# Optimization experiments

Hardware: AMD Instinct MI355X
Metric: run time of the kernel (lower is better)

Reference implementation:

```python
import jax, jax.numpy as jnp
import numpy as np

B, S, H, NH, E, D = 2, 2048, 1024, 16, 8, 1024
HD = H // NH
EPS = 1e-5


def act_quant(x):
    # BitNet b1.58 per-row (last axis) int8 activation quant with STE
    s = 127.0 / jnp.clip(jnp.max(jnp.abs(x), axis=-1, keepdims=True), 1e-5, None)
    q = jnp.clip(jnp.round(x * s), -128, 127) / s
    return x + jax.lax.stop_gradient(q - x)


def w_quant(w, axes=None):
    # ternary weight quant (mean-abs scale) with STE; axes=None -> whole tensor
    s = 1.0 / jnp.clip(jnp.mean(jnp.abs(w), axis=axes, keepdims=axes is not None), 1e-5, None)
    q = jnp.clip(jnp.round(w * s), -1, 1) / s
    return w + jax.lax.stop_gradient(q - w)


def bitlinear(x, w):  # x [..., I], w [O, I] (torch layout)
    return act_quant(x) @ w_quant(w).T


def rmsnorm(x, w):
    return x * jax.lax.rsqrt(jnp.mean(x * x, axis=-1, keepdims=True) + EPS) * w


def setup_inputs() -> dict:
    key = jax.random.key(0)
    ks = jax.random.split(key, 10)
    def n(k, shape, scale=0.02):
        return jax.random.normal(k, shape, jnp.float32) * scale
    return {
        "x": jax.random.normal(ks[0], (B, S, H), jnp.float32),
        "q_w": n(ks[1], (H, H)),
        "k_w": n(ks[2], (H, H)),
        "v_w": n(ks[3], (H, H)),
        "o_w": n(ks[4], (H, H)),
        "ln1_w": jnp.ones((H,), jnp.float32),
        "ln2_w": jnp.ones((H,), jnp.float32),
        "router_w": n(ks[5], (E, H)),
        "gate_w": n(ks[6], (E, D, H)),
        "up_w": n(ks[7], (E, D, H)),
        "down_w": n(ks[8], (E, H, D)),
    }


def reference(x, q_w, k_w, v_w, o_w, ln1_w, ln2_w, router_w, gate_w, up_w, down_w):
    # ---- attention (BitNet projections, manual causal softmax) ----
    residual = x
    xn = rmsnorm(x, ln1_w)
    q = bitlinear(xn, q_w).reshape(B, S, NH, HD).transpose(0, 2, 1, 3)  # [B,NH,S,HD]
    k = bitlinear(xn, k_w).reshape(B, S, NH, HD).transpose(0, 2, 1, 3)
    v = bitlinear(xn, v_w).reshape(B, S, NH, HD).transpose(0, 2, 1, 3)
    scale = 1.0 / jnp.sqrt(jnp.asarray(HD, x.dtype))
    attn = jnp.einsum('bhqd,bhkd->bhqk', q, k) * scale
    causal = jnp.triu(jnp.ones((S, S), bool), k=1)
    attn = jnp.where(causal[None, None], -jnp.inf, attn)
    attn = jax.nn.softmax(attn, axis=-1)
    h = jnp.einsum('bhqk,bhkd->bhqd', attn, v).transpose(0, 2, 1, 3).reshape(B, S, H)
    x = residual + bitlinear(h, o_w)

    # ---- top-1 MoE (BitNet experts, relu^2 glu) ----
    residual = x
    xn = rmsnorm(x, ln2_w)
    xf = xn.reshape(-1, H)                       # [T, H], T = B*S
    logits = xf @ router_w.T                     # [T, E]
    idx = jnp.argmax(logits, axis=-1)            # [T]
    onehot = jax.nn.one_hot(idx, E, dtype=x.dtype)  # [T, E]

    xq = act_quant(xf)
    gw = w_quant(gate_w, axes=(1, 2))            # per-expert ternary
    uw = w_quant(up_w, axes=(1, 2))
    dw = w_quant(down_w, axes=(1, 2))
    g = jnp.einsum('th,edh->etd', xq, gw)        # [E, T, D]
    u = jnp.einsum('th,edh->etd', xq, uw)
    hh = jnp.square(jnp.maximum(g, 0)) * u       # relu(gate)^2 * up
    o = jnp.einsum('etd,ehd->eth', act_quant(hh), dw)  # [E, T, H]
    moe = jnp.einsum('eth,te->th', o, onehot).reshape(B, S, H)

    return residual + moe
```

## Files before the change

### kernel.cpp

```cpp
#include <hip/hip_runtime.h>
#include <stdint.h>
#include <math.h>

#define NTOK 4096
#define H    1024
#define NHEAD 16
#define HD   64
#define SEQ  2048
#define NE   8
#define DDIM 1024

typedef __attribute__((ext_vector_type(4)))  int i32x4;
typedef __attribute__((ext_vector_type(16))) int i32x16;
typedef __attribute__((ext_vector_type(8)))  short bf16x8;
typedef __attribute__((ext_vector_type(4)))  float f32x4;


__device__ __forceinline__ i32x16 mfma_i8(i32x4 a, i32x4 b, i32x16 c) {
  return __builtin_amdgcn_mfma_i32_32x32x32_i8(a, b, c, 0, 0, 0);
}

__device__ __forceinline__ unsigned int f2bf(float f) {
  unsigned int u = __float_as_uint(f);
  return (u + 0x7fffu + ((u >> 16) & 1u)) >> 16;
}
__device__ __forceinline__ float bf2f(unsigned int b) {
  return __uint_as_float(b << 16);
}
__device__ __forceinline__ unsigned int f2bf2hl(float a, float b, unsigned int& lo) {
  unsigned int ha = f2bf(a), hb = f2bf(b);
  lo = f2bf(a - bf2f(ha)) | (f2bf(b - bf2f(hb)) << 16);
  return ha | (hb << 16);
}
__device__ __forceinline__ unsigned int fpair(float a) {
  unsigned int hi = f2bf(a);
  unsigned int lo = f2bf(a - bf2f(hi));
  return hi | (lo << 16);
}
__device__ __forceinline__ unsigned int ror16(unsigned int x) {
  return (x >> 16) | (x << 16);
}

__device__ __forceinline__ double bredd(double v, int op, double* tmp) {
#pragma unroll
  for (int o = 32; o; o >>= 1) {
    double w = __shfl_xor(v, o);
    v = op ? fmax(v, w) : v + w;
  }
  int wid = threadIdx.x >> 6;
  if ((threadIdx.x & 63) == 0) tmp[wid] = v;
  __syncthreads();
  double r = op ? fmax(fmax(tmp[0], tmp[1]), fmax(tmp[2], tmp[3]))
                : (tmp[0] + tmp[1] + tmp[2] + tmp[3]);
  __syncthreads();
  return r;
}

__device__ __forceinline__ int qpackd(double n0, double n1, double n2, double n3, double s) {
  int a = (int)fmin(fmax(rint(n0 * s), -128.0), 127.0);
  int b = (int)fmin(fmax(rint(n1 * s), -128.0), 127.0);
  int c = (int)fmin(fmax(rint(n2 * s), -128.0), 127.0);
  int d = (int)fmin(fmax(rint(n3 * s), -128.0), 127.0);
  return (a & 255) | ((b & 255) << 8) | ((c & 255) << 16) | ((d & 255) << 24);
}

__device__ __forceinline__ const float* wsrc(int tensor,
    const float* qw_, const float* kw_, const float* vw_, const float* ow_,
    const float* gw_, const float* uw_, const float* dw_) {
  if (tensor < 4) return tensor == 0 ? qw_ : tensor == 1 ? kw_ : tensor == 2 ? vw_ : ow_;
  if (tensor < 12) return gw_ + ((long long)(tensor - 4) << 20);
  if (tensor < 20) return uw_ + ((long long)(tensor - 12) << 20);
  return dw_ + ((long long)(tensor - 20) << 20);
}


__global__ __launch_bounds__(256) void k_absum(
    const float* qw_, const float* kw_, const float* vw_, const float* ow_,
    const float* gw_, const float* uw_, const float* dw_, double* partial) {
  __shared__ double tmp[4];
  int tensor = blockIdx.x >> 10;
  int j = ((blockIdx.x & 1023) << 10) + threadIdx.x * 4;
  const float* src = wsrc(tensor, qw_, kw_, vw_, ow_, gw_, uw_, dw_);
  float4 w = *(const float4*)(src + j);
  double v = fabs((double)w.x) + fabs((double)w.y) + fabs((double)w.z) + fabs((double)w.w);
  v = bredd(v, 0, tmp);
  if (threadIdx.x == 0) partial[blockIdx.x] = v;
}

__global__ __launch_bounds__(256) void k_wscale(const double* partial, double* wsd) {
  __shared__ double tmp[4];
  int tensor = blockIdx.x;
  const double* p = partial + (tensor << 10);
  int i = threadIdx.x * 4;
  double v = p[i] + p[i + 1] + p[i + 2] + p[i + 3];
  v = bredd(v, 0, tmp);
  if (threadIdx.x == 0) wsd[tensor] = 1.0 / fmax(v * (1.0 / 1048576.0), 1e-5);
}

__global__ __launch_bounds__(256) void k_quantw(
    const float* qw_, const float* kw_, const float* vw_, const float* ow_,
    const float* gw_, const float* uw_, const float* dw_,
    const double* wsd, int8_t* qw) {
  int tensor = blockIdx.x >> 10;
  int j = ((blockIdx.x & 1023) << 10) + threadIdx.x * 4;
  const float* src = wsrc(tensor, qw_, kw_, vw_, ow_, gw_, uw_, dw_);
  double s = wsd[tensor];
  float4 w = *(const float4*)(src + j);
  int a = (int)fmin(fmax(rint((double)w.x * s), -1.0), 1.0);
  int b = (int)fmin(fmax(rint((double)w.y * s), -1.0), 1.0);
  int c = (int)fmin(fmax(rint((double)w.z * s), -1.0), 1.0);
  int d = (int)fmin(fmax(rint((double)w.w * s), -1.0), 1.0);
  ((int*)qw)[(tensor << 18) + (j >> 2)] =
      (a & 255) | ((b & 255) << 8) | ((c & 255) << 16) | ((d & 255) << 24);
}


__global__ __launch_bounds__(256) void k_rms1(const float* X, const float* lnw,
                                              int8_t* xq, double* xsd) {
  __shared__ double tmp[4];
  int t = blockIdx.x, tid = threadIdx.x;
  float4 xv = ((const float4*)(X + (long long)t * H))[tid];
  double x0 = xv.x, x1 = xv.y, x2 = xv.z, x3 = xv.w;
  double ss = x0 * x0 + x1 * x1 + x2 * x2 + x3 * x3;
  ss = bredd(ss, 0, tmp);
  double r = 1.0 / sqrt(ss * (1.0 / 1024.0) + 1e-5);
  float4 wv = ((const float4*)lnw)[tid];
  double n0 = x0 * r * wv.x, n1 = x1 * r * wv.y, n2 = x2 * r * wv.z, n3 = x3 * r * wv.w;
  double ma = fmax(fmax(fabs(n0), fabs(n1)), fmax(fabs(n2), fabs(n3)));
  ma = bredd(ma, 1, tmp);
  double s = 127.0 / fmax(ma, 1e-5);
  ((int*)xq)[t * 256 + tid] = qpackd(n0, n1, n2, n3, s);
  if (tid == 0) xsd[t] = s;
}

__global__ __launch_bounds__(256) void k_actq(const float* X, int8_t* xq, double* xsd) {
  __shared__ double tmp[4];
  int t = blockIdx.x, tid = threadIdx.x;
  float4 xv = ((const float4*)(X + (long long)t * H))[tid];
  double x0 = xv.x, x1 = xv.y, x2 = xv.z, x3 = xv.w;
  double ma = fmax(fmax(fabs(x0), fabs(x1)), fmax(fabs(x2), fabs(x3)));
  ma = bredd(ma, 1, tmp);
  double s = 127.0 / fmax(ma, 1e-5);
  ((int*)xq)[t * 256 + tid] = qpackd(x0, x1, x2, x3, s);
  if (tid == 0) xsd[t] = s;
}


__global__ __launch_bounds__(256) void k_gemm(
    const int8_t* __restrict__ Xq, const double* __restrict__ xsd,
    const int8_t* __restrict__ W, const double* __restrict__ wsd, int widx,
    const float* __restrict__ residual, float* __restrict__ out) {
  __shared__ i32x4 Xs[4][64];
  __shared__ i32x4 Ws[4][128];
  __shared__ double invs[64];
  int tid = threadIdx.x;
  int t0 = blockIdx.y * 64, n0 = blockIdx.x * 128;
  int w = tid >> 6, lane = tid & 63;
  int lrow = lane & 31, lk = lane >> 5;
  int xrow = tid >> 2, xkc = tid & 3;
  i32x16 acc[2];
#pragma unroll
  for (int i = 0; i < 2; i++)
#pragma unroll
    for (int r = 0; r < 16; r++) acc[i][r] = 0;

  for (int k0 = 0; k0 < 1024; k0 += 64) {
    Xs[xkc][xrow] = *(const i32x4*)(Xq + (long long)(t0 + xrow) * 1024 + k0 + xkc * 16);
#pragma unroll
    for (int i = 0; i < 2; i++) {
      int u = tid * 2 + i;
      int row = u >> 2, kc = u & 3;
      Ws[kc][row] = *(const i32x4*)(W + (long long)(n0 + row) * 1024 + k0 + kc * 16);
    }
    __syncthreads();
#pragma unroll
    for (int ks = 0; ks < 2; ks++) {
      i32x4 a0 = Xs[ks * 2 + lk][lrow];
      i32x4 a1 = Xs[ks * 2 + lk][32 + lrow];
      i32x4 b  = Ws[ks * 2 + lk][w * 32 + lrow];
      acc[0] = mfma_i8(a0, b, acc[0]);
      acc[1] = mfma_i8(a1, b, acc[1]);
    }
    __syncthreads();
  }

  double sw = wsd[widx];
  if (tid < 64) invs[tid] = 1.0 / (xsd[t0 + tid] * sw);
  __syncthreads();
  int n = n0 + w * 32 + lrow;
#pragma unroll
  for (int i = 0; i < 2; i++) {
#pragma unroll
    for (int r = 0; r < 16; r++) {
      int rl = i * 32 + (r & 3) + 8 * (r >> 2) + 4 * lk;
      int trow = t0 + rl;
      double v = (double)acc[i][r] * invs[rl];
      if (residual) v += (double)residual[(long long)trow * H + n];
      out[(long long)trow * H + n] = (float)v;
    }
  }
}


__global__ __launch_bounds__(256) void k_gemm3(
    const int8_t* __restrict__ Xq, const double* __restrict__ xsd,
    const int8_t* __restrict__ qw, const double* __restrict__ wsd,
    float* __restrict__ outq, unsigned short* __restrict__ Kh,
    unsigned short* __restrict__ Kl, unsigned int* __restrict__ Vp) {
  __shared__ i32x4 Xs[4][128];
  __shared__ i32x4 Ws[4][128];
  __shared__ double invs[128];
  int z = blockIdx.z;
  const int8_t* W = qw + ((long long)z << 20);
  int tid = threadIdx.x;
  int t0 = blockIdx.y * 128, n0 = blockIdx.x * 128;
  int w = tid >> 6, lane = tid & 63;
  int wm = w >> 1, wn = w & 1;
  int lrow = lane & 31, lk = lane >> 5;
  i32x16 acc[2][2];
#pragma unroll
  for (int i = 0; i < 2; i++)
#pragma unroll
    for (int j = 0; j < 2; j++)
#pragma unroll
      for (int r = 0; r < 16; r++) acc[i][j][r] = 0;

  for (int k0 = 0; k0 < 1024; k0 += 64) {
#pragma unroll
    for (int i = 0; i < 2; i++) {
      int u = tid * 2 + i;
      int row = u >> 2, kc = u & 3;
      Xs[kc][row] = *(const i32x4*)(Xq + (long long)(t0 + row) * 1024 + k0 + kc * 16);
      Ws[kc][row] = *(const i32x4*)(W  + (long long)(n0 + row) * 1024 + k0 + kc * 16);
    }
    __syncthreads();
#pragma unroll
    for (int ks = 0; ks < 2; ks++) {
      i32x4 a0 = Xs[ks * 2 + lk][wm * 64 + lrow];
      i32x4 a1 = Xs[ks * 2 + lk][wm * 64 + 32 + lrow];
      i32x4 b0 = Ws[ks * 2 + lk][wn * 64 + lrow];
      i32x4 b1 = Ws[ks * 2 + lk][wn * 64 + 32 + lrow];
      acc[0][0] = mfma_i8(a0, b0, acc[0][0]);
      acc[0][1] = mfma_i8(a0, b1, acc[0][1]);
      acc[1][0] = mfma_i8(a1, b0, acc[1][0]);
      acc[1][1] = mfma_i8(a1, b1, acc[1][1]);
    }
    __syncthreads();
  }

  double sw = wsd[z];
  if (tid < 128) invs[tid] = 1.0 / (xsd[t0 + tid] * sw);
  __syncthreads();
#pragma unroll
  for (int i = 0; i < 2; i++) {
#pragma unroll
    for (int r = 0; r < 16; r++) {
      int rloc = wm * 64 + i * 32 + (r & 3) + 8 * (r >> 2) + 4 * lk;
      long long base = (long long)(t0 + rloc) * H;
      double inv = invs[rloc];
#pragma unroll
      for (int j = 0; j < 2; j++) {
        int n = n0 + wn * 64 + j * 32 + lrow;
        float vf = (float)((double)acc[i][j][r] * inv);
        long long idx = base + n;
        if (z == 0) {
          outq[idx] = vf;
        } else if (z == 1) {
          unsigned int h = f2bf(vf);
          unsigned int l = f2bf(vf - bf2f(h));
          Kh[idx] = (unsigned short)h;
          Kl[idx] = (unsigned short)l;
        } else {
          Vp[idx] = fpair(vf);
        }
      }
    }
  }
}


__global__ __launch_bounds__(256) void k_knorm(const unsigned short* __restrict__ Kh,
                                               const unsigned short* __restrict__ Kl,
                                               float* __restrict__ Mk) {
  __shared__ float tmp[4];
  int bh = blockIdx.x;
  int b = bh >> 4, head = bh & 15;
  int tid = threadIdx.x;
  float mx = 0.f;
  for (int key = tid; key < SEQ; key += 256) {
    long long base = ((long long)(b * SEQ + key)) * H + head * HD;
    const uint4* hq4 = (const uint4*)(Kh + base);
    const uint4* lq4 = (const uint4*)(Kl + base);
    float s = 0.f;
#pragma unroll
    for (int i = 0; i < 8; i++) {
      uint4 hu = hq4[i], lu = lq4[i];
      const unsigned int hw[4] = {hu.x, hu.y, hu.z, hu.w};
      const unsigned int lw[4] = {lu.x, lu.y, lu.z, lu.w};
#pragma unroll
      for (int j = 0; j < 4; j++) {
        float v0 = bf2f(hw[j] & 0xffffu) + bf2f(lw[j] & 0xffffu);
        float v1 = bf2f(hw[j] >> 16)     + bf2f(lw[j] >> 16);
        s += v0 * v0 + v1 * v1;
      }
    }
    mx = fmaxf(mx, s);
  }
#pragma unroll
  for (int o = 32; o; o >>= 1) mx = fmaxf(mx, __shfl_xor(mx, o));
  if ((tid & 63) == 0) tmp[tid >> 6] = mx;
  __syncthreads();
  if (tid == 0)
    Mk[bh] = sqrtf(fmaxf(fmaxf(tmp[0], tmp[1]), fmaxf(tmp[2], tmp[3])));
}


__global__ __launch_bounds__(512, 4) void k_attn(
    const float* __restrict__ Q, const unsigned short* __restrict__ KH,
    const unsigned short* __restrict__ KL, const unsigned int* __restrict__ VP,
    float* __restrict__ O, const float* __restrict__ Mk) {
  __shared__ unsigned short Qb[64][72];
  __shared__ unsigned short Ql[64][72];
  __shared__ unsigned short Kb[64][72];
  __shared__ unsigned short Kl[64][72];
  __shared__ unsigned int   VA[64][76];
  __shared__ unsigned int   Pw[64][76];
  __shared__ float mbs[64];
  __shared__ float lsh[8][16];
  int i = blockIdx.x;
  int hb = (i & 7) | (((i >> 3) & 3) << 3);
  int p  = ((i >> 5) & 7) | (((i >> 8) & 1) << 3);
  int head = hb & 15, b = hb >> 4;
  int tid = threadIdx.x;
  int w = tid >> 6, lane = tid & 63;
  int quad = lane >> 2, dp = lane & 3;
  int d0 = dp << 4;
  int l15 = lane & 15, lhi = lane >> 4;
  int qh = w >> 2, ks = w & 3;
  long long bh_base = ((long long)b * SEQ) * H + head * HD;
  float mkv = Mk[b * 16 + head];

  int srow = tid >> 3;
  int sd = (tid & 7) << 3;
  int vswz = (tid & 7) << 2;

  int qb = w >> 1;

  for (int ph = 0; ph < 2; ph++) {
    int g = ph ? (31 - p) : p;
    int qlo = g * 64;

    {
      const float* qg = Q + bh_base + (long long)(qlo + srow) * H + sd;
      float4 a = *(const float4*)qg;
      float4 c = *(const float4*)(qg + 4);
      uint4 phh, pll;
      phh.x = f2bf2hl(a.x * 0.125f, a.y * 0.125f, pll.x);
      phh.y = f2bf2hl(a.z * 0.125f, a.w * 0.125f, pll.y);
      phh.z = f2bf2hl(c.x * 0.125f, c.y * 0.125f, pll.z);
      phh.w = f2bf2hl(c.z * 0.125f, c.w * 0.125f, pll.w);
      *(uint4*)&Qb[srow][sd] = phh;
      *(uint4*)&Ql[srow][sd] = pll;
    }

    if (ks == 0) {
      int j0 = qh * 32 + quad * 2;
#pragma unroll
      for (int qq = 0; qq < 2; qq++) {
        int j = j0 + qq;
        const float4* qp_ = (const float4*)(Q + bh_base + (long long)(qlo + j) * H + d0);
        float ss = 0.f;
#pragma unroll
        for (int i2 = 0; i2 < 4; i2++) {
          float4 t = qp_[i2];
          ss += t.x * t.x + t.y * t.y + t.z * t.z + t.w * t.w;
        }
        ss += __shfl_xor(ss, 1);
        ss += __shfl_xor(ss, 2);
        if (dp == 0) mbs[j] = 0.125f * sqrtf(ss) * mkv;
      }
    }

    float lp[4] = {0.f, 0.f, 0.f, 0.f};
    f32x4 oacc[2];
#pragma unroll
    for (int fi = 0; fi < 2; fi++)
#pragma unroll
      for (int r = 0; r < 4; r++) oacc[fi][r] = 0.f;

    __syncthreads();

    bf16x8 qah[2], qal[2];
#pragma unroll
    for (int ks2 = 0; ks2 < 2; ks2++) {
      qah[ks2] = *(const bf16x8*)&Qb[qb * 16 + l15][ks2 * 32 + lhi * 8];
      qal[ks2] = *(const bf16x8*)&Ql[qb * 16 + l15][ks2 * 32 + lhi * 8];
    }
    float mbr4[4];
#pragma unroll
    for (int r = 0; r < 4; r++) mbr4[r] = mbs[qb * 16 + lhi * 4 + r];

    for (int t = 0; t <= g; t++) {
      {
        long long idx = bh_base + (long long)(t * 64 + srow) * H + sd;
        *(uint4*)&Kb[srow][sd] = *(const uint4*)(KH + idx);
        *(uint4*)&Kl[srow][sd] = *(const uint4*)(KL + idx);
        const uint4* vg = (const uint4*)(VP + idx);
        uint4 va = vg[0], vb = vg[1];
        int col = srow ^ vswz;
        VA[sd + 0][col] = va.x;
        VA[sd + 1][col] = va.y;
        VA[sd + 2][col] = va.z;
        VA[sd + 3][col] = va.w;
        VA[sd + 4][col] = vb.x;
        VA[sd + 5][col] = vb.y;
        VA[sd + 6][col] = vb.z;
        VA[sd + 7][col] = vb.w;
      }
      __syncthreads();

      {
        bool dg = (t == g);
#pragma unroll
        for (int kb2 = 0; kb2 < 2; kb2++) {
          int kb = (w & 1) * 2 + kb2;
          f32x4 c = {0.f, 0.f, 0.f, 0.f};
          __builtin_amdgcn_s_setprio(1);
#pragma unroll
          for (int ks2 = 0; ks2 < 2; ks2++) {
            bf16x8 bh = *(const bf16x8*)&Kb[kb * 16 + l15][ks2 * 32 + lhi * 8];
            bf16x8 bl = *(const bf16x8*)&Kl[kb * 16 + l15][ks2 * 32 + lhi * 8];
            c = __builtin_amdgcn_mfma_f32_16x16x32_bf16(qal[ks2], bh, c, 0, 0, 0);
            c = __builtin_amdgcn_mfma_f32_16x16x32_bf16(qah[ks2], bl, c, 0, 0, 0);
            c = __builtin_amdgcn_mfma_f32_16x16x32_bf16(qah[ks2], bh, c, 0, 0, 0);
          }
          __builtin_amdgcn_s_setprio(0);
          int colc = kb * 16 + l15;
#pragma unroll
          for (int r = 0; r < 4; r++) {
            int row = qb * 16 + lhi * 4 + r;
            float wgt = (dg && colc > row) ? 0.f : __expf(c[r] - mbr4[r]);
            lp[r] += wgt;
            Pw[row][colc] = fpair(wgt);
          }
        }
      }
      __syncthreads();

      __builtin_amdgcn_s_setprio(1);
#pragma unroll
      for (int c4 = 0; c4 < 4; c4++) {
        bf16x8 af = *(const bf16x8*)&Pw[qb * 16 + l15][c4 * 16 + lhi * 4];
#pragma unroll
        for (int fi = 0; fi < 2; fi++) {
          int d4 = (w * 2 + fi) & 3;
          int row = d4 * 16 + l15;
          int rswz = ((row >> 3) & 7) << 2;
          union { uint4 q; unsigned int u[4]; bf16x8 v; } bb, bs;
          bb.q = *(const uint4*)&VA[row][(c4 * 16 + lhi * 4) ^ rswz];
          oacc[fi] = __builtin_amdgcn_mfma_f32_16x16x32_bf16(af, bb.v, oacc[fi], 0, 0, 0);
#pragma unroll
          for (int j = 0; j < 4; j++)
            bs.u[j] = ror16(bb.u[j]);
          oacc[fi] = __builtin_amdgcn_mfma_f32_16x16x32_bf16(af, bs.v, oacc[fi], 0, 0, 0);
        }
      }
      __builtin_amdgcn_s_setprio(0);
      __syncthreads();
    }

#pragma unroll
    for (int r = 0; r < 4; r++) {
      lp[r] += __shfl_xor(lp[r], 1);
      lp[r] += __shfl_xor(lp[r], 2);
      lp[r] += __shfl_xor(lp[r], 4);
      lp[r] += __shfl_xor(lp[r], 8);
    }
    if (l15 == 0) {
#pragma unroll
      for (int r = 0; r < 4; r++) lsh[w][lhi * 4 + r] = lp[r];
    }
    __syncthreads();

#pragma unroll
    for (int fi = 0; fi < 2; fi++) {
      int f = w * 2 + fi;
      int d4 = f & 3;
#pragma unroll
      for (int r = 0; r < 4; r++) {
        int idx = lhi * 4 + r;
        float lt = lsh[qb * 2][idx] + lsh[qb * 2 + 1][idx];
        float inv = 1.f / lt;
        int qrow = qb * 16 + idx;
        O[bh_base + (long long)(qlo + qrow) * H + d4 * 16 + l15] = oacc[fi][r] * inv;
      }
    }
    __syncthreads();
  }
}


__global__ __launch_bounds__(256) void k_rms2_router(
    const float* X2, const float* lnw, const float* rw,
    int8_t* xq, double* xsd, int* eidx) {
  __shared__ double tmp[4];
  __shared__ double xn[1024];
  __shared__ double logits[8];
  int t = blockIdx.x, tid = threadIdx.x;
  float4 xv = ((const float4*)(X2 + (long long)t * H))[tid];
  double x0 = xv.x, x1 = xv.y, x2 = xv.z, x3 = xv.w;
  double ss = x0 * x0 + x1 * x1 + x2 * x2 + x3 * x3;
  ss = bredd(ss, 0, tmp);
  double r = 1.0 / sqrt(ss * (1.0 / 1024.0) + 1e-5);
  float4 wv = ((const float4*)lnw)[tid];
  double n0 = x0 * r * wv.x, n1 = x1 * r * wv.y, n2 = x2 * r * wv.z, n3 = x3 * r * wv.w;
  xn[tid * 4 + 0] = n0; xn[tid * 4 + 1] = n1;
  xn[tid * 4 + 2] = n2; xn[tid * 4 + 3] = n3;
  double ma = fmax(fmax(fabs(n0), fabs(n1)), fmax(fabs(n2), fabs(n3)));
  ma = bredd(ma, 1, tmp);
  double s = 127.0 / fmax(ma, 1e-5);
  ((int*)xq)[t * 256 + tid] = qpackd(n0, n1, n2, n3, s);
  if (tid == 0) xsd[t] = s;
  if (tid < 64) {
    int e = tid >> 3, i = tid & 7;
    const float* wr = rw + e * 1024;
    double p = 0.0;
    for (int h = i; h < 1024; h += 8) p += xn[h] * (double)wr[h];
    p += __shfl_xor(p, 1);
    p += __shfl_xor(p, 2);
    p += __shfl_xor(p, 4);
    if (i == 0) logits[e] = p;
  }
  __syncthreads();
  if (tid == 0) {
    double best = logits[0];
    int bi = 0;
    for (int e = 1; e < 8; e++)
      if (logits[e] > best) { best = logits[e]; bi = e; }
    eidx[t] = bi;
  }
}


__global__ __launch_bounds__(256) void k_route(const int* __restrict__ eidx,
                                               int* __restrict__ meta,
                                               int* __restrict__ tokidx) {
  __shared__ int cnt[8], pb[9], cur[8];
  int tid = threadIdx.x;
  if (tid < 8) cnt[tid] = 0;
  __syncthreads();
  for (int t = tid; t < NTOK; t += 256) atomicAdd(&cnt[eidx[t]], 1);
  __syncthreads();
  if (tid == 0) {
    pb[0] = 0;
    int nt = 0;
    for (int e = 0; e < 8; e++) {
      int tiles = (cnt[e] + 63) >> 6;
      for (int i = 0; i < tiles; i++) meta[1 + nt + i] = e;
      nt += tiles;
      pb[e + 1] = pb[e] + tiles * 64;
      cur[e] = pb[e];
    }
    meta[0] = nt;
  }
  __syncthreads();
  for (int s = tid; s < 4608; s += 256) tokidx[s] = -1;
  __syncthreads();
  for (int t = tid; t < NTOK; t += 256) {
    int e = eidx[t];
    int s = atomicAdd(&cur[e], 1);
    tokidx[s] = t;
  }
}


__global__ __launch_bounds__(256) void k_moe_gu(
    const int8_t* __restrict__ Xq, const double* __restrict__ xsd,
    const int8_t* __restrict__ qw, const double* __restrict__ wsd,
    const int* __restrict__ meta, const int* __restrict__ tokidx,
    float* __restrict__ hhbuf) {
  __shared__ i32x4 Xs[4][64];
  __shared__ i32x4 Wg[4][128];
  __shared__ i32x4 Wu[4][128];
  __shared__ double invg[64], invu[64];
  int tile = blockIdx.y;
  if (tile >= meta[0]) return;
  int e = meta[1 + tile];
  int n0 = blockIdx.x * 128;
  int s0 = tile * 64;
  int tid = threadIdx.x;
  int w = tid >> 6, lane = tid & 63;
  int lrow = lane & 31, lk = lane >> 5;
  const int8_t* Gg = qw + ((long long)(4 + e) << 20);
  const int8_t* Ug = qw + ((long long)(12 + e) << 20);
  int xrow = tid >> 2, xkc = tid & 3;
  int tokr = tokidx[s0 + xrow];
  if (tokr < 0) tokr = 0;
  i32x16 accg[2], accu[2];
#pragma unroll
  for (int i = 0; i < 2; i++)
#pragma unroll
    for (int r = 0; r < 16; r++) { accg[i][r] = 0; accu[i][r] = 0; }

  for (int k0 = 0; k0 < 1024; k0 += 64) {
    Xs[xkc][xrow] = *(const i32x4*)(Xq + (long long)tokr * 1024 + k0 + xkc * 16);
#pragma unroll
    for (int i = 0; i < 2; i++) {
      int u = tid * 2 + i;
      int row = u >> 2, kc = u & 3;
      Wg[kc][row] = *(const i32x4*)(Gg + (long long)(n0 + row) * 1024 + k0 + kc * 16);
      Wu[kc][row] = *(const i32x4*)(Ug + (long long)(n0 + row) * 1024 + k0 + kc * 16);
    }
    __syncthreads();
#pragma unroll
    for (int ks = 0; ks < 2; ks++) {
      i32x4 a0 = Xs[ks * 2 + lk][lrow];
      i32x4 a1 = Xs[ks * 2 + lk][32 + lrow];
      i32x4 bg = Wg[ks * 2 + lk][w * 32 + lrow];
      i32x4 bu = Wu[ks * 2 + lk][w * 32 + lrow];
      accg[0] = mfma_i8(a0, bg, accg[0]);
      accg[1] = mfma_i8(a1, bg, accg[1]);
      accu[0] = mfma_i8(a0, bu, accu[0]);
      accu[1] = mfma_i8(a1, bu, accu[1]);
    }
    __syncthreads();
  }

  double swg = wsd[4 + e], swu = wsd[12 + e];
  if (tid < 64) {
    int tk = tokidx[s0 + tid];
    double xs = (tk < 0) ? 1.0 : xsd[tk];
    invg[tid] = 1.0 / (xs * swg);
    invu[tid] = 1.0 / (xs * swu);
  }
  __syncthreads();
  int n = n0 + w * 32 + lrow;
#pragma unroll
  for (int i = 0; i < 2; i++) {
#pragma unroll
    for (int r = 0; r < 16; r++) {
      int sl = i * 32 + (r & 3) + 8 * (r >> 2) + 4 * lk;
      int s = s0 + sl;
      int tok = tokidx[s];
      if (tok < 0) continue;
      double g = (double)accg[i][r] * invg[sl];
      double uu = (double)accu[i][r] * invu[sl];
      double rg = fmax(g, 0.0);
      hhbuf[(long long)s * DDIM + n] = (float)(rg * rg * uu);
    }
  }
}


__global__ __launch_bounds__(256) void k_hh_actq(
    const float* __restrict__ hhbuf, const int* __restrict__ meta,
    const int* __restrict__ tokidx, int8_t* __restrict__ hq,
    double* __restrict__ hsd) {
  __shared__ double tmp[4];
  int s = blockIdx.x;
  if (s >= meta[0] * 64) return;
  int tid = threadIdx.x;
  int tok = tokidx[s];
  if (tok < 0) {
    ((int*)hq)[s * 256 + tid] = 0;
    if (tid == 0) hsd[s] = 1.0;
    return;
  }
  float4 xv = ((const float4*)(hhbuf + (long long)s * DDIM))[tid];
  double x0 = xv.x, x1 = xv.y, x2 = xv.z, x3 = xv.w;
  double ma = fmax(fmax(fabs(x0), fabs(x1)), fmax(fabs(x2), fabs(x3)));
  ma = bredd(ma, 1, tmp);
  double sc = 127.0 / fmax(ma, 1e-5);
  ((int*)hq)[s * 256 + tid] = qpackd(x0, x1, x2, x3, sc);
  if (tid == 0) hsd[s] = sc;
}


__global__ __launch_bounds__(256) void k_moe_down(
    const int8_t* __restrict__ hq, const double* __restrict__ hsd,
    const int8_t* __restrict__ qw, const double* __restrict__ wsd,
    const int* __restrict__ meta, const int* __restrict__ tokidx,
    const float* __restrict__ x2, float* __restrict__ out) {
  __shared__ i32x4 Xs[4][64];
  __shared__ i32x4 Ws[4][128];
  __shared__ double invd[64];
  int tile = blockIdx.y;
  if (tile >= meta[0]) return;
  int e = meta[1 + tile];
  int n0 = blockIdx.x * 128;
  int s0 = tile * 64;
  int tid = threadIdx.x;
  int w = tid >> 6, lane = tid & 63;
  int lrow = lane & 31, lk = lane >> 5;
  const int8_t* Wp = qw + ((long long)(20 + e) << 20);
  int xrow = tid >> 2, xkc = tid & 3;
  i32x16 acc[2];
#pragma unroll
  for (int i = 0; i < 2; i++)
#pragma unroll
    for (int r = 0; r < 16; r++) acc[i][r] = 0;

  for (int k0 = 0; k0 < 1024; k0 += 64) {
    Xs[xkc][xrow] = *(const i32x4*)(hq + (long long)(s0 + xrow) * 1024 + k0 + xkc * 16);
#pragma unroll
    for (int i = 0; i < 2; i++) {
      int u = tid * 2 + i;
      int row = u >> 2, kc = u & 3;
      Ws[kc][row] = *(const i32x4*)(Wp + (long long)(n0 + row) * 1024 + k0 + kc * 16);
    }
    __syncthreads();
#pragma unroll
    for (int ks = 0; ks < 2; ks++) {
      i32x4 a0 = Xs[ks * 2 + lk][lrow];
      i32x4 a1 = Xs[ks * 2 + lk][32 + lrow];
      i32x4 b  = Ws[ks * 2 + lk][w * 32 + lrow];
      acc[0] = mfma_i8(a0, b, acc[0]);
      acc[1] = mfma_i8(a1, b, acc[1]);
    }
    __syncthreads();
  }

  double sw = wsd[20 + e];
  if (tid < 64) invd[tid] = 1.0 / (hsd[s0 + tid] * sw);
  __syncthreads();
  int n = n0 + w * 32 + lrow;
#pragma unroll
  for (int i = 0; i < 2; i++) {
#pragma unroll
    for (int r = 0; r < 16; r++) {
      int sl = i * 32 + (r & 3) + 8 * (r >> 2) + 4 * lk;
      int s = s0 + sl;
      int tok = tokidx[s];
      if (tok < 0) continue;
      out[(long long)tok * H + n] =
          (float)((double)x2[(long long)tok * H + n] + (double)acc[i][r] * invd[sl]);
    }
  }
}

extern "C" void kernel_launch(void* const* d_in, const int* in_sizes, int n_in,
                              void* d_out, int out_size, void* d_ws, size_t ws_size,
                              hipStream_t stream) {
  const float* x   = (const float*)d_in[0];
  const float* qw_ = (const float*)d_in[1];
  const float* kw_ = (const float*)d_in[2];
  const float* vw_ = (const float*)d_in[3];
  const float* ow_ = (const float*)d_in[4];
  const float* ln1 = (const float*)d_in[5];
  const float* ln2 = (const float*)d_in[6];
  const float* rw  = (const float*)d_in[7];
  const float* gw  = (const float*)d_in[8];
  const float* uw  = (const float*)d_in[9];
  const float* dw  = (const float*)d_in[10];
  float* out = (float*)d_out;

  uint8_t* ws = (uint8_t*)d_ws;
  double* partial = (double*)ws;
  double* wsd    = (double*)(ws + 229376);
  double* xsd    = (double*)(ws + 229600);
  int*    eidx   = (int*)(ws + 262368);
  float*  Mk     = (float*)(ws + 278752);
  int*    meta   = (int*)(ws + 278912);
  int*    tokidx = (int*)(ws + 279424);
  double* hsd    = (double*)(ws + 297856);
  int8_t* qw     = (int8_t*)(ws + (1ull << 20));
  int8_t* xq     = (int8_t*)(ws + (29ull << 20));
  float*  qbuf   = (float*)(ws + (33ull << 20));
  float*  hhbuf  = (float*)(ws + (33ull << 20));
  unsigned short* Kh = (unsigned short*)(ws + (49ull << 20));
  unsigned short* Kl = (unsigned short*)(ws + (57ull << 20));
  int8_t* hq     = (int8_t*)(ws + (52ull << 20));
  unsigned int* Vp = (unsigned int*)(ws + (65ull << 20));
  float*  vbuf   = (float*)(ws + (65ull << 20));

  k_absum<<<28 * 1024, 256, 0, stream>>>(qw_, kw_, vw_, ow_, gw, uw, dw, partial);
  k_wscale<<<28, 256, 0, stream>>>(partial, wsd);
  k_quantw<<<28 * 1024, 256, 0, stream>>>(qw_, kw_, vw_, ow_, gw, uw, dw, wsd, qw);

  k_rms1<<<NTOK, 256, 0, stream>>>(x, ln1, xq, xsd);
  k_gemm3<<<dim3(8, 32, 3), 256, 0, stream>>>(xq, xsd, qw, wsd, qbuf, Kh, Kl, Vp);
  k_knorm<<<32, 256, 0, stream>>>(Kh, Kl, Mk);
  k_attn<<<dim3(512), 512, 0, stream>>>(qbuf, Kh, Kl, Vp, qbuf, Mk);
  k_actq<<<NTOK, 256, 0, stream>>>(qbuf, xq, xsd);
  k_gemm<<<dim3(8, 64), 256, 0, stream>>>(xq, xsd, qw + (3 << 20), wsd, 3, x, vbuf);
  k_rms2_router<<<NTOK, 256, 0, stream>>>(vbuf, ln2, rw, xq, xsd, eidx);
  k_route<<<1, 256, 0, stream>>>(eidx, meta, tokidx);
  k_moe_gu<<<dim3(8, 71), 256, 0, stream>>>(xq, xsd, qw, wsd, meta, tokidx, hhbuf);
  k_hh_actq<<<4544, 256, 0, stream>>>(hhbuf, meta, tokidx, hq, hsd);
  k_moe_down<<<dim3(8, 71), 256, 0, stream>>>(hq, hsd, qw, wsd, meta, tokidx, vbuf, out);
}
```

Before: 463.5 us.

## Prefetch next K/V tile into registers and use exp2 with folded log2e scale

The attention loop now loads the next K/V tile from global memory into registers right after the barrier, so the fetch overlaps with the current tile's MFMA and softmax work instead of stalling before the LDS store. The Q scale and the max bound are also multiplied by log2(e), so the softmax weights can use the native exp2 instruction instead of __expf. This adds register pressure, which may lower occupancy, and slightly changes rounding because the scale is folded into the bf16 hi/lo split of Q.

```diff
diff --git a/kernel.cpp b/kernel.cpp
--- a/kernel.cpp
+++ b/kernel.cpp
@@ -14,6 +14,8 @@
 typedef __attribute__((ext_vector_type(16))) int i32x16;
 typedef __attribute__((ext_vector_type(8)))  short bf16x8;
 typedef __attribute__((ext_vector_type(4)))  float f32x4;
+
+#define LOG2E 1.4426950408889634f
 
 
 __device__ __forceinline__ i32x16 mfma_i8(i32x4 a, i32x4 b, i32x16 c) {
@@ -346,6 +348,8 @@
 
   int qb = w >> 1;
 
+  const float qscale = 0.125f * LOG2E;
+
   for (int ph = 0; ph < 2; ph++) {
     int g = ph ? (31 - p) : p;
     int qlo = g * 64;
@@ -355,10 +359,10 @@
       float4 a = *(const float4*)qg;
       float4 c = *(const float4*)(qg + 4);
       uint4 phh, pll;
-      phh.x = f2bf2hl(a.x * 0.125f, a.y * 0.125f, pll.x);
-      phh.y = f2bf2hl(a.z * 0.125f, a.w * 0.125f, pll.y);
-      phh.z = f2bf2hl(c.x * 0.125f, c.y * 0.125f, pll.z);
-      phh.w = f2bf2hl(c.z * 0.125f, c.w * 0.125f, pll.w);
+      phh.x = f2bf2hl(a.x * qscale, a.y * qscale, pll.x);
+      phh.y = f2bf2hl(a.z * qscale, a.w * qscale, pll.y);
+      phh.z = f2bf2hl(c.x * qscale, c.y * qscale, pll.z);
+      phh.w = f2bf2hl(c.z * qscale, c.w * qscale, pll.w);
       *(uint4*)&Qb[srow][sd] = phh;
       *(uint4*)&Ql[srow][sd] = pll;
     }
@@ -377,7 +381,7 @@
         }
         ss += __shfl_xor(ss, 1);
         ss += __shfl_xor(ss, 2);
-        if (dp == 0) mbs[j] = 0.125f * sqrtf(ss) * mkv;
+        if (dp == 0) mbs[j] = qscale * sqrtf(ss) * mkv;
       }
     }
 
@@ -400,24 +404,40 @@
 #pragma unroll
     for (int r = 0; r < 4; r++) mbr4[r] = mbs[qb * 16 + lhi * 4 + r];
 
+    uint4 kh_r, kl_r, vp_r0, vp_r1;
+    {
+      long long idx = bh_base + (long long)(srow) * H + sd;
+      kh_r = *(const uint4*)(KH + idx);
+      kl_r = *(const uint4*)(KL + idx);
+      const uint4* vg = (const uint4*)(VP + idx);
+      vp_r0 = vg[0];
+      vp_r1 = vg[1];
+    }
+
     for (int t = 0; t <= g; t++) {
       {
-        long long idx = bh_base + (long long)(t * 64 + srow) * H + sd;
-        *(uint4*)&Kb[srow][sd] = *(const uint4*)(KH + idx);
-        *(uint4*)&Kl[srow][sd] = *(const uint4*)(KL + idx);
-        const uint4* vg = (const uint4*)(VP + idx);
-        uint4 va = vg[0], vb = vg[1];
+        *(uint4*)&Kb[srow][sd] = kh_r;
+        *(uint4*)&Kl[srow][sd] = kl_r;
         int col = srow ^ vswz;
-        VA[sd + 0][col] = va.x;
-        VA[sd + 1][col] = va.y;
-        VA[sd + 2][col] = va.z;
-        VA[sd + 3][col] = va.w;
-        VA[sd + 4][col] = vb.x;
-        VA[sd + 5][col] = vb.y;
-        VA[sd + 6][col] = vb.z;
-        VA[sd + 7][col] = vb.w;
+        VA[sd + 0][col] = vp_r0.x;
+        VA[sd + 1][col] = vp_r0.y;
+        VA[sd + 2][col] = vp_r0.z;
+        VA[sd + 3][col] = vp_r0.w;
+        VA[sd + 4][col] = vp_r1.x;
+        VA[sd + 5][col] = vp_r1.y;
+        VA[sd + 6][col] = vp_r1.z;
+        VA[sd + 7][col] = vp_r1.w;
       }
       __syncthreads();
+
+      if (t < g) {
+        long long idx = bh_base + (long long)((t + 1) * 64 + srow) * H + sd;
+        kh_r = *(const uint4*)(KH + idx);
+        kl_r = *(const uint4*)(KL + idx);
+        const uint4* vg = (const uint4*)(VP + idx);
+        vp_r0 = vg[0];
+        vp_r1 = vg[1];
+      }
 
       {
         bool dg = (t == g);
@@ -439,7 +459,8 @@
 #pragma unroll
           for (int r = 0; r < 4; r++) {
             int row = qb * 16 + lhi * 4 + r;
-            float wgt = (dg && colc > row) ? 0.f : __expf(c[r] - mbr4[r]);
+            float wgt = (dg && colc > row) ? 0.f
+                        : __builtin_amdgcn_exp2f(c[r] - mbr4[r]);
             lp[r] += wgt;
             Pw[row][colc] = fpair(wgt);
           }
```

Result: no change. 460.5 us (median of 2 runs) (-0.6%).
